# Performance work log

Measured on AMD Instinct MI355X. Metric: run time of the kernel, lower is better.

The kernel has to match this reference:

```python
import jax, jax.numpy as jnp
import numpy as np

B, Q, C, NH, NL, NP, DFF = 8, 300, 256, 8, 4, 4, 1024
DH = C // NH
SHAPES = [(100, 100), (50, 50), (25, 25), (13, 13)]  # (H, W) per level
LEN = sum(h * w for h, w in SHAPES)


def _ln(x, g, b):
    m = x.mean(-1, keepdims=True)
    v = ((x - m) ** 2).mean(-1, keepdims=True)
    return (x - m) / jnp.sqrt(v + 1e-5) * g + b


def _bilinear(v, loc, H, W):
    # v: [B, NH, H*W, DH]; loc: [B, NH, Q, NP, 2] normalized to [0,1]
    # grid_sample(align_corners=False, padding_mode='zeros') semantics
    x = loc[..., 0] * W - 0.5
    y = loc[..., 1] * H - 0.5
    x0 = jnp.floor(x)
    y0 = jnp.floor(y)
    dx = x - x0
    dy = y - y0
    out = jnp.zeros(x.shape + (v.shape[-1],), v.dtype)
    for xi, yi, wgt in ((x0, y0, (1 - dx) * (1 - dy)),
                        (x0 + 1, y0, dx * (1 - dy)),
                        (x0, y0 + 1, (1 - dx) * dy),
                        (x0 + 1, y0 + 1, dx * dy)):
        valid = ((xi >= 0) & (xi < W) & (yi >= 0) & (yi < H)).astype(v.dtype)
        idx = jnp.clip(yi, 0, H - 1).astype(jnp.int32) * W + jnp.clip(xi, 0, W - 1).astype(jnp.int32)
        g = jnp.take_along_axis(v, idx.reshape(idx.shape[0], idx.shape[1], -1)[..., None], axis=2)
        out = out + (wgt * valid)[..., None] * g.reshape(x.shape + (v.shape[-1],))
    return out


def _forward(tgt, reference_points, memory, query_pos_embed,
             Wq, bq, Wk, bk, Wv, bv, Wo, bo, g1, be1,
             W_off, b_off, W_attn, b_attn, W_val, b_val, W_out, b_out, g2, be2,
             W1, b1, W2, b2, g3, be3):
    scale = 1.0 / float(np.sqrt(DH))
    # ---- self attention (q = k = tgt + pos, v = tgt) ----
    qk = tgt + query_pos_embed
    q = (qk @ Wq + bq).reshape(B, Q, NH, DH)
    k = (qk @ Wk + bk).reshape(B, Q, NH, DH)
    v = (tgt @ Wv + bv).reshape(B, Q, NH, DH)
    attn = jax.nn.softmax(jnp.einsum('bqhd,bkhd->bhqk', q, k) * scale, axis=-1)
    sa = jnp.einsum('bhqk,bkhd->bqhd', attn, v).reshape(B, Q, C) @ Wo + bo
    t = _ln(tgt + sa, g1, be1)
    # ---- multi-scale deformable cross attention ----
    query = t + query_pos_embed
    value = (memory @ W_val + b_val).reshape(B, LEN, NH, DH).transpose(0, 2, 1, 3)  # [B,NH,LEN,DH]
    off = (query @ W_off + b_off).reshape(B, Q, NH, NL, NP, 2)
    aw = jax.nn.softmax((query @ W_attn + b_attn).reshape(B, Q, NH, NL * NP), axis=-1)
    aw = aw.reshape(B, Q, NH, NL, NP)
    wh = jnp.array([[w, h] for h, w in SHAPES], jnp.float32)  # offset normalizer (W, H)
    loc = reference_points[:, :, None, :, None, :] + off / wh[None, None, None, :, None, :]
    out = jnp.zeros((B, NH, Q, DH), t.dtype)
    start = 0
    for l, (h, w) in enumerate(SHAPES):
        v_l = value[:, :, start:start + h * w]
        loc_l = loc[:, :, :, l].transpose(0, 2, 1, 3, 4)  # [B,NH,Q,NP,2]
        samp = _bilinear(v_l, loc_l, h, w)                # [B,NH,Q,NP,DH]
        out = out + (samp * aw[:, :, :, l].transpose(0, 2, 1, 3)[..., None]).sum(3)
        start += h * w
    ca = out.transpose(0, 2, 1, 3).reshape(B, Q, C) @ W_out + b_out
    t = _ln(t + ca, g2, be2)
    # ---- FFN ----
    ff = jax.nn.relu(t @ W1 + b1) @ W2 + b2
    return _ln(t + ff, g3, be3)


def setup_inputs() -> dict:
    ks = jax.random.split(jax.random.key(0), 16)
    z, o = jnp.zeros, jnp.ones
    w = lambda i, sh: jax.random.normal(ks[i], sh, jnp.float32) * 0.02
    return {
        'tgt': jax.random.normal(ks[0], (B, Q, C), jnp.float32),
        'reference_points': jax.random.uniform(ks[1], (B, Q, NL, 2), jnp.float32),
        'memory': jax.random.normal(ks[2], (B, LEN, C), jnp.float32),
        'query_pos_embed': jax.random.normal(ks[3], (B, Q, C), jnp.float32),
        'Wq': w(4, (C, C)), 'bq': z(C), 'Wk': w(5, (C, C)), 'bk': z(C),
        'Wv': w(6, (C, C)), 'bv': z(C), 'Wo': w(7, (C, C)), 'bo': z(C),
        'g1': o(C), 'be1': z(C),
        'W_off': w(8, (C, NH * NL * NP * 2)), 'b_off': z(NH * NL * NP * 2),
        'W_attn': w(9, (C, NH * NL * NP)), 'b_attn': z(NH * NL * NP),
        'W_val': w(10, (C, C)), 'b_val': z(C), 'W_out': w(11, (C, C)), 'b_out': z(C),
        'g2': o(C), 'be2': z(C),
        'W1': w(12, (C, DFF)), 'b1': z(DFF), 'W2': w(13, (DFF, C)), 'b2': z(C),
        'g3': o(C), 'be3': z(C),
        'spatial_shapes': jnp.array(SHAPES, jnp.int32),
        'level_start_index': jnp.array(np.cumsum([0] + [h * w for h, w in SHAPES[:-1]]), jnp.int32),
    }


def reference(tgt, reference_points, memory, query_pos_embed,
              Wq, bq, Wk, bk, Wv, bv, Wo, bo, g1, be1,
              W_off, b_off, W_attn, b_attn, W_val, b_val, W_out, b_out, g2, be2,
              W1, b1, W2, b2, g3, be3, spatial_shapes, level_start_index):
    return _forward(tgt, reference_points, memory, query_pos_embed,
                    Wq, bq, Wk, bk, Wv, bv, Wo, bo, g1, be1,
                    W_off, b_off, W_attn, b_attn, W_val, b_val, W_out, b_out, g2, be2,
                    W1, b1, W2, b2, g3, be3)
```

## Files before the change

kernel.cpp:

```cpp
#include <hip/hip_runtime.h>
#include <hip/hip_bf16.h>
#include <math.h>

#define B_   8
#define Q_   300
#define C_   256
#define NH_  8
#define NL_  4
#define NP_  4
#define DFF_ 1024
#define DH_  32
#define LEN_ 13294
#define MQ_  (B_*Q_)
#define MV_  (B_*LEN_)
#define NSTRIP_ 3324

typedef __attribute__((ext_vector_type(4))) float f32x4;
typedef __attribute__((ext_vector_type(8))) short bf16x8;
typedef __hip_bfloat16 bf16;

#define GLOAD16(gp, lp) __builtin_amdgcn_global_load_lds( \
    (const __attribute__((address_space(1))) unsigned int*)(gp), \
    (__attribute__((address_space(3))) unsigned int*)(lp), 16, 0, 0)

__device__ __forceinline__ short f2bfbits(float x) {
    bf16 h = __float2bfloat16(x);
    return *reinterpret_cast<short*>(&h);
}

__global__ __launch_bounds__(256) void k_dualcvt(const float* __restrict__ tgt,
                                                 const float* __restrict__ qpe,
                                                 bf16* __restrict__ qk_o,
                                                 bf16* __restrict__ tgt_o, int n8) {
    int i = blockIdx.x * 256 + threadIdx.x;
    if (i >= n8) return;
    const float4* pa = (const float4*)(tgt + (size_t)i * 8);
    const float4* pb = (const float4*)(qpe + (size_t)i * 8);
    float4 x = pa[0], y = pa[1], u = pb[0], w = pb[1];
    union { bf16 h[8]; uint4 v; } s, t;
    s.h[0] = __float2bfloat16(x.x + u.x); s.h[1] = __float2bfloat16(x.y + u.y);
    s.h[2] = __float2bfloat16(x.z + u.z); s.h[3] = __float2bfloat16(x.w + u.w);
    s.h[4] = __float2bfloat16(y.x + w.x); s.h[5] = __float2bfloat16(y.y + w.y);
    s.h[6] = __float2bfloat16(y.z + w.z); s.h[7] = __float2bfloat16(y.w + w.w);
    t.h[0] = __float2bfloat16(x.x); t.h[1] = __float2bfloat16(x.y);
    t.h[2] = __float2bfloat16(x.z); t.h[3] = __float2bfloat16(x.w);
    t.h[4] = __float2bfloat16(y.x); t.h[5] = __float2bfloat16(y.y);
    t.h[6] = __float2bfloat16(y.z); t.h[7] = __float2bfloat16(y.w);
    *(uint4*)(qk_o + (size_t)i * 8)  = s.v;
    *(uint4*)(tgt_o + (size_t)i * 8) = t.v;
}

__global__ __launch_bounds__(256) void k_wtall(
        const float* __restrict__ Wq, const float* __restrict__ Wk,
        const float* __restrict__ Wv, const float* __restrict__ Wo,
        const float* __restrict__ Wval, const float* __restrict__ Woff,
        const float* __restrict__ Wattn, const float* __restrict__ Wout,
        const float* __restrict__ W1, const float* __restrict__ W2,
        bf16* __restrict__ Wqk_t, bf16* __restrict__ Wv_t, bf16* __restrict__ Wo_t,
        bf16* __restrict__ Wval_t, bf16* __restrict__ Woa_t, bf16* __restrict__ Wout_t,
        bf16* __restrict__ W1_t, bf16* __restrict__ W2_t) {
    __shared__ float t[32][33];
    const int id = blockIdx.x;
    const float* W; bf16* D; int K, N, r;
    if      (id < 64)  { W = Wq;    D = Wqk_t;          K = 256;  N = 256;  r = id; }
    else if (id < 128) { W = Wk;    D = Wqk_t + 65536;  K = 256;  N = 256;  r = id - 64; }
    else if (id < 192) { W = Wv;    D = Wv_t;           K = 256;  N = 256;  r = id - 128; }
    else if (id < 256) { W = Wo;    D = Wo_t;           K = 256;  N = 256;  r = id - 192; }
    else if (id < 320) { W = Wval;  D = Wval_t;         K = 256;  N = 256;  r = id - 256; }
    else if (id < 384) { W = Woff;  D = Woa_t;          K = 256;  N = 256;  r = id - 320; }
    else if (id < 416) { W = Wattn; D = Woa_t + 65536;  K = 256;  N = 128;  r = id - 384; }
    else if (id < 480) { W = Wout;  D = Wout_t;         K = 256;  N = 256;  r = id - 416; }
    else if (id < 736) { W = W1;    D = W1_t;           K = 256;  N = 1024; r = id - 480; }
    else               { W = W2;    D = W2_t;           K = 1024; N = 256;  r = id - 736; }
    const int nx = N >> 5;
    const int k0 = (r / nx) * 32, n0 = (r % nx) * 32;
    const int c = threadIdx.x & 31, rr = threadIdx.x >> 5;
#pragma unroll
    for (int i = 0; i < 4; ++i)
        t[rr + i * 8][c] = W[(size_t)(k0 + rr + i * 8) * N + n0 + c];
    __syncthreads();
#pragma unroll
    for (int i = 0; i < 4; ++i)
        D[(size_t)(n0 + rr + i * 8) * K + k0 + c] = __float2bfloat16(t[c][rr + i * 8]);
}

__global__ __launch_bounds__(256, 2) void k_gmmV(const float* __restrict__ A,
                                                 const bf16* __restrict__ Bt,
                                                 const float* __restrict__ bias,
                                                 bf16* __restrict__ outh,
                                                 int M) {
    __shared__ short As[2][8 * 32 * 32];
    const int tid = threadIdx.x;
    const int w = tid >> 6, lane = tid & 63;
    const int fr = lane & 15, fq = lane >> 4;
    const int r   = tid >> 3;
    const int itc = tid & 7;

    bf16x8 bc[4][8];
#pragma unroll
    for (int n = 0; n < 4; ++n)
#pragma unroll
        for (int it = 0; it < 8; ++it)
            bc[n][it] = *(const bf16x8*)(Bt + (size_t)(w * 64 + n * 16 + fr) * 256 + it * 32 + fq * 8);
    float bs[4];
#pragma unroll
    for (int n = 0; n < 4; ++n) bs[n] = bias[w * 64 + n * 16 + fr];

    const int sbase = blockIdx.x * 4;
    float4 pf[8];

#define LOADA(s_) { \
        int row_ = (s_) * 32 + r; if (row_ > M - 1) row_ = M - 1; \
        const float4* p_ = (const float4*)(A + (size_t)row_ * 256 + itc * 32); \
        pf[0] = p_[0]; pf[1] = p_[1]; pf[2] = p_[2]; pf[3] = p_[3]; \
        pf[4] = p_[4]; pf[5] = p_[5]; pf[6] = p_[6]; pf[7] = p_[7]; }
#define WRITEA(buf_) { \
        short* dst_ = &As[buf_][itc * 1024 + r * 32]; \
        _Pragma("unroll") \
        for (int g_ = 0; g_ < 4; ++g_) { \
            float4 a0_ = pf[2 * g_], a1_ = pf[2 * g_ + 1]; \
            union { short h[8]; bf16x8 v; } cv_; \
            cv_.h[0] = f2bfbits(a0_.x); cv_.h[1] = f2bfbits(a0_.y); \
            cv_.h[2] = f2bfbits(a0_.z); cv_.h[3] = f2bfbits(a0_.w); \
            cv_.h[4] = f2bfbits(a1_.x); cv_.h[5] = f2bfbits(a1_.y); \
            cv_.h[6] = f2bfbits(a1_.z); cv_.h[7] = f2bfbits(a1_.w); \
            *(bf16x8*)(dst_ + g_ * 8) = cv_.v; \
        } }

    LOADA(sbase);
    WRITEA(0);
    __syncthreads();
    int buf = 0;
#pragma unroll 1
    for (int i = 0; i < 4; ++i) {
        const int s = sbase + i;
        if (s >= NSTRIP_) break;
        const bool more = (i < 3) && (s + 1 < NSTRIP_);
        if (more) LOADA(s + 1);
        f32x4 acc[2][4] = {};
#pragma unroll
        for (int it = 0; it < 8; ++it) {
            bf16x8 af[2];
#pragma unroll
            for (int m = 0; m < 2; ++m)
                af[m] = *(const bf16x8*)&As[buf][it * 1024 + (m * 16 + fr) * 32 + fq * 8];
#pragma unroll
            for (int m = 0; m < 2; ++m)
#pragma unroll
                for (int n = 0; n < 4; ++n)
                    acc[m][n] = __builtin_amdgcn_mfma_f32_16x16x32_bf16(af[m], bc[n][it], acc[m][n], 0, 0, 0);
        }
        if (more) WRITEA(buf ^ 1);
#pragma unroll
        for (int m = 0; m < 2; ++m)
#pragma unroll
            for (int n = 0; n < 4; ++n) {
                const int c = w * 64 + n * 16 + fr;
#pragma unroll
                for (int j = 0; j < 4; ++j) {
                    const int row = s * 32 + m * 16 + fq * 4 + j;
                    if (row < M)
                        outh[(size_t)row * 256 + c] = __float2bfloat16(acc[m][n][j] + bs[n]);
                }
            }
        if (more) __syncthreads();
        buf ^= 1;
    }
#undef LOADA
#undef WRITEA
}

template<int RELU, int OUT_MODE>
__global__ __launch_bounds__(256) void k_gmm64(const bf16* __restrict__ A,
                                               const bf16* __restrict__ Bt,
                                               const float* __restrict__ bias0,
                                               const float* __restrict__ bias1,
                                               int nsplit,
                                               float* __restrict__ outf,
                                               bf16* __restrict__ outh,
                                               int M, int N, int K) {
    __shared__ bf16 As[64 * 32];
    __shared__ bf16 Bs[64 * 32];
    const int tid  = threadIdx.x;
    const int wid  = tid >> 6, lane = tid & 63;
    const int m0 = blockIdx.y * 64, n0 = blockIdx.x * 64;
    const int wr = wid >> 1, wc = wid & 1;
    const int fr = lane & 15, fq = lane >> 4;
    const int rloc = wid * 16 + (lane >> 2);
    const int kof  = (lane & 3) * 8;
    f32x4 acc[2][2] = {};
    for (int k0 = 0; k0 < K; k0 += 32) {
        if (k0) __syncthreads();
        int gr = m0 + rloc; if (gr > M - 1) gr = M - 1;
        GLOAD16(A + (size_t)gr * K + k0 + kof, As + rloc * 32);
        int gc = n0 + rloc; if (gc > N - 1) gc = N - 1;
        GLOAD16(Bt + (size_t)gc * K + k0 + kof, Bs + rloc * 32);
        __syncthreads();
        bf16x8 af[2], bfr[2];
#pragma unroll
        for (int m = 0; m < 2; ++m)
            af[m] = *(const bf16x8*)(As + (wr * 32 + m * 16 + fr) * 32 + fq * 8);
#pragma unroll
        for (int n = 0; n < 2; ++n)
            bfr[n] = *(const bf16x8*)(Bs + (wc * 32 + n * 16 + fr) * 32 + fq * 8);
#pragma unroll
        for (int m = 0; m < 2; ++m)
#pragma unroll
            for (int n = 0; n < 2; ++n)
                acc[m][n] = __builtin_amdgcn_mfma_f32_16x16x32_bf16(af[m], bfr[n], acc[m][n], 0, 0, 0);
    }
#pragma unroll
    for (int m = 0; m < 2; ++m) {
#pragma unroll
        for (int n = 0; n < 2; ++n) {
            const int c = n0 + wc * 32 + n * 16 + fr;
            const float bs = (c < nsplit) ? bias0[c] : bias1[c - nsplit];
#pragma unroll
            for (int j = 0; j < 4; ++j) {
                const int r = m0 + wr * 32 + m * 16 + fq * 4 + j;
                if (r >= M) continue;
                float v = acc[m][n][j] + bs;
                if (RELU) v = fmaxf(v, 0.f);
                if (OUT_MODE == 0) outf[(size_t)r * N + c] = v;
                else               outh[(size_t)r * N + c] = __float2bfloat16(v);
            }
        }
    }
}

__global__ __launch_bounds__(256) void k_attn(const bf16* __restrict__ qk2,
                                              const bf16* __restrict__ vb,
                                              bf16* __restrict__ sa) {
    __shared__ short Ks[304][40];
    __shared__ short Vt[32][328];
    __shared__ short Ps[4][16][168];
    const int tid = threadIdx.x, w = tid >> 6, lane = tid & 63;
    const int fr = lane & 15, fq = lane >> 4;
    const int bh = blockIdx.y, b = bh >> 3, h = bh & 7;
    const int qbase = blockIdx.x * 64;

    for (int k0 = 0; k0 < 300; k0 += 64) {
        int key = k0 + (tid >> 2);
        int dc = (tid & 3) * 8;
        if (key < 300) {
            *(bf16x8*)&Ks[key][dc] =
                *(const bf16x8*)&qk2[((size_t)(b * 300 + key)) * 512 + 256 + h * 32 + dc];
            bf16x8 v8 = *(const bf16x8*)&vb[((size_t)(b * 300 + key)) * 256 + h * 32 + dc];
#pragma unroll
            for (int i = 0; i < 8; ++i) Vt[dc + i][key] = v8[i];
        }
    }
    for (int i = tid; i < 32 * 20; i += 256) Vt[i & 31][300 + (i >> 5)] = 0;

    int qrow = qbase + w * 16 + fr;
    int qr = qrow < 300 ? qrow : 299;
    bf16x8 qf = *(const bf16x8*)&qk2[((size_t)(b * 300 + qr)) * 512 + h * 32 + fq * 8];
    __syncthreads();

    f32x4 s[19];
#pragma unroll
    for (int kf = 0; kf < 19; ++kf) {
        bf16x8 kfr = *(const bf16x8*)&Ks[kf * 16 + fr][fq * 8];
        f32x4 z = {};
        s[kf] = __builtin_amdgcn_mfma_f32_16x16x32_bf16(qf, kfr, z, 0, 0, 0);
    }
    const float scale = 0.17677669529663687f;
#pragma unroll
    for (int kf = 0; kf < 19; ++kf)
#pragma unroll
        for (int j = 0; j < 4; ++j) s[kf][j] *= scale;
    if (288 + fr >= 300) {
#pragma unroll
        for (int j = 0; j < 4; ++j) s[18][j] = -1e30f;
    }
    float mx[4], sm[4], inv[4];
#pragma unroll
    for (int j = 0; j < 4; ++j) {
        mx[j] = s[0][j];
#pragma unroll
        for (int kf = 1; kf < 19; ++kf) mx[j] = fmaxf(mx[j], s[kf][j]);
    }
#pragma unroll
    for (int off = 1; off < 16; off <<= 1)
#pragma unroll
        for (int j = 0; j < 4; ++j) mx[j] = fmaxf(mx[j], __shfl_xor(mx[j], off));
#pragma unroll
    for (int j = 0; j < 4; ++j) sm[j] = 0.f;
#pragma unroll
    for (int kf = 0; kf < 19; ++kf)
#pragma unroll
        for (int j = 0; j < 4; ++j) { s[kf][j] = expf(s[kf][j] - mx[j]); sm[j] += s[kf][j]; }
#pragma unroll
    for (int off = 1; off < 16; off <<= 1)
#pragma unroll
        for (int j = 0; j < 4; ++j) sm[j] += __shfl_xor(sm[j], off);
#pragma unroll
    for (int j = 0; j < 4; ++j) inv[j] = 1.f / sm[j];

    f32x4 o[2] = {};
#pragma unroll
    for (int half = 0; half < 2; ++half) {
        const int kfbeg = half * 10, kfend = half ? 19 : 10;
#pragma unroll
        for (int kf = kfbeg; kf < kfend; ++kf) {
            int gcol = kf * 16 + fr, lcol = gcol - half * 160;
            bool valid = gcol < 300;
#pragma unroll
            for (int j = 0; j < 4; ++j)
                Ps[w][fq * 4 + j][lcol] = valid ? f2bfbits(s[kf][j] * inv[j]) : (short)0;
        }
        if (half) {
            int r = lane >> 2, c0 = 144 + (lane & 3) * 4;
#pragma unroll
            for (int i = 0; i < 4; ++i) Ps[w][r][c0 + i] = 0;
        }
#pragma unroll
        for (int ks = 0; ks < 5; ++ks) {
            bf16x8 pa = *(const bf16x8*)&Ps[w][fr][ks * 32 + fq * 8];
#pragma unroll
            for (int n = 0; n < 2; ++n) {
                bf16x8 vf = *(const bf16x8*)&Vt[n * 16 + fr][half * 160 + ks * 32 + fq * 8];
                o[n] = __builtin_amdgcn_mfma_f32_16x16x32_bf16(pa, vf, o[n], 0, 0, 0);
            }
        }
    }
#pragma unroll
    for (int n = 0; n < 2; ++n)
#pragma unroll
        for (int j = 0; j < 4; ++j) {
            int row = qbase + w * 16 + fq * 4 + j;
            if (row < 300)
                sa[((size_t)(b * 300 + row)) * 256 + h * 32 + n * 16 + fr] = __float2bfloat16(o[n][j]);
        }
}

template<int WB>
__global__ __launch_bounds__(256) void k_ln(const float* __restrict__ x,
                                            const float* __restrict__ res,
                                            const float* __restrict__ qpe,
                                            const float* __restrict__ g,
                                            const float* __restrict__ be,
                                            float* __restrict__ out,
                                            bf16* __restrict__ outh, int rows) {
    const int row = blockIdx.x;
    const int tid = threadIdx.x;
    float v = x[row * C_ + tid] + res[row * C_ + tid];
    __shared__ float red[4];
    float s = v;
#pragma unroll
    for (int off = 32; off; off >>= 1) s += __shfl_xor(s, off);
    if ((tid & 63) == 0) red[tid >> 6] = s;
    __syncthreads();
    float mean = (red[0] + red[1] + red[2] + red[3]) * (1.f / C_);
    float dv = v - mean;
    float s2 = dv * dv;
    __syncthreads();
#pragma unroll
    for (int off = 32; off; off >>= 1) s2 += __shfl_xor(s2, off);
    if ((tid & 63) == 0) red[tid >> 6] = s2;
    __syncthreads();
    float var = (red[0] + red[1] + red[2] + red[3]) * (1.f / C_);
    float rstd = 1.f / sqrtf(var + 1e-5f);
    float y = dv * rstd * g[tid] + be[tid];
    out[row * C_ + tid] = y;
    if (WB == 1) outh[row * C_ + tid] = __float2bfloat16(y);
    if (WB == 2) outh[row * C_ + tid] = __float2bfloat16(y + qpe[row * C_ + tid]);
}

__global__ __launch_bounds__(256) void k_sample(const bf16* __restrict__ value,
                                                const float* __restrict__ refp,
                                                const float* __restrict__ offaw,
                                                bf16* __restrict__ out) {
    const int t  = blockIdx.x * 256 + threadIdx.x;
    const int d2 = t & 15;
    const int g  = t >> 4;
    const int h  = g & 7;
    const int bq = g >> 3;
    const int b  = bq / Q_;
    const int starts[4] = {0, 10000, 12500, 13125};
    const int HW[4]     = {100, 50, 25, 13};
    const float* offp = offaw + (size_t)bq * 384 + h * 32;

    float myl = offaw[(size_t)bq * 384 + 256 + h * 16 + d2];
    float mxl = myl;
#pragma unroll
    for (int o = 1; o < 16; o <<= 1) mxl = fmaxf(mxl, __shfl_xor(mxl, o));
    float e = expf(myl - mxl);
    float se = e;
#pragma unroll
    for (int o = 1; o < 16; o <<= 1) se += __shfl_xor(se, o);
    const float myaw = e / se;

    float acc0 = 0.f, acc1 = 0.f;
#pragma unroll
    for (int l = 0; l < NL_; ++l) {
        const int Hl = HW[l], Wl = HW[l], st = starts[l];
        const float rx = refp[(bq * NL_ + l) * 2 + 0];
        const float ry = refp[(bq * NL_ + l) * 2 + 1];
        const bf16* vbase = value + ((size_t)b * LEN_ + st) * C_ + h * DH_ + d2 * 2;
#pragma unroll
        for (int p = 0; p < NP_; ++p) {
            const float ox = offp[l * 8 + p * 2 + 0];
            const float oy = offp[l * 8 + p * 2 + 1];
            const float x = (rx + ox / (float)Wl) * (float)Wl - 0.5f;
            const float y = (ry + oy / (float)Hl) * (float)Hl - 0.5f;
            const float x0 = floorf(x), y0 = floorf(y);
            const float dx = x - x0, dy = y - y0;
            const int ix0 = (int)x0, iy0 = (int)y0;
            const float aw = __shfl(myaw, l * 4 + p, 16);
            float s0 = 0.f, s1 = 0.f;
#pragma unroll
            for (int cor = 0; cor < 4; ++cor) {
                const int xi = ix0 + (cor & 1), yi = iy0 + (cor >> 1);
                if (xi >= 0 && xi < Wl && yi >= 0 && yi < Hl) {
                    const float wg = (cor & 1 ? dx : 1.f - dx) * (cor >> 1 ? dy : 1.f - dy);
                    const unsigned u = *(const unsigned*)(vbase + (size_t)(yi * Wl + xi) * C_);
                    bf16 lo, hi;
                    *reinterpret_cast<short*>(&lo) = (short)(u & 0xFFFF);
                    *reinterpret_cast<short*>(&hi) = (short)(u >> 16);
                    s0 += wg * __bfloat162float(lo);
                    s1 += wg * __bfloat162float(hi);
                }
            }
            acc0 += aw * s0;
            acc1 += aw * s1;
        }
    }
    union { short h2[2]; unsigned u; } pack;
    pack.h2[0] = f2bfbits(acc0);
    pack.h2[1] = f2bfbits(acc1);
    *(unsigned*)(out + (size_t)bq * C_ + h * DH_ + d2 * 2) = pack.u;
}

extern "C" void kernel_launch(void* const* d_in, const int* in_sizes, int n_in,
                              void* d_out, int out_size, void* d_ws, size_t ws_size,
                              hipStream_t stream) {
    const float* tgt    = (const float*)d_in[0];
    const float* refp   = (const float*)d_in[1];
    const float* memory = (const float*)d_in[2];
    const float* qpe    = (const float*)d_in[3];
    const float* Wq     = (const float*)d_in[4];  const float* bq_  = (const float*)d_in[5];
    const float* Wk     = (const float*)d_in[6];  const float* bk_  = (const float*)d_in[7];
    const float* Wv     = (const float*)d_in[8];  const float* bv_  = (const float*)d_in[9];
    const float* Wo     = (const float*)d_in[10]; const float* bo_  = (const float*)d_in[11];
    const float* g1     = (const float*)d_in[12]; const float* be1  = (const float*)d_in[13];
    const float* W_off  = (const float*)d_in[14]; const float* b_off  = (const float*)d_in[15];
    const float* W_attn = (const float*)d_in[16]; const float* b_attn = (const float*)d_in[17];
    const float* W_val  = (const float*)d_in[18]; const float* b_val  = (const float*)d_in[19];
    const float* W_out  = (const float*)d_in[20]; const float* b_out  = (const float*)d_in[21];
    const float* g2     = (const float*)d_in[22]; const float* be2  = (const float*)d_in[23];
    const float* W1     = (const float*)d_in[24]; const float* b1   = (const float*)d_in[25];
    const float* W2     = (const float*)d_in[26]; const float* b2   = (const float*)d_in[27];
    const float* g3     = (const float*)d_in[28]; const float* be3  = (const float*)d_in[29];
    float* out = (float*)d_out;

    char* base = (char*)d_ws;
    size_t off = 0;
    auto alloc = [&](size_t bytes) -> char* {
        char* p = base + off; off = (off + bytes + 255) & ~(size_t)255; return p;
    };
    float* t1       = (float*)alloc(MQ_ * C_ * 4);
    float* offaw    = (float*)alloc((size_t)MQ_ * 384 * 4);
    bf16*  query_bf = (bf16*) alloc(MQ_ * C_ * 2);
    bf16*  dsout_bf = (bf16*) alloc(MQ_ * C_ * 2);
    bf16*  Wqk_t  = (bf16*)alloc(512 * C_ * 2);
    bf16*  Wv_t   = (bf16*)alloc(C_ * C_ * 2);
    bf16*  Wo_t   = (bf16*)alloc(C_ * C_ * 2);
    bf16*  Wval_t = (bf16*)alloc(C_ * C_ * 2);
    bf16*  Woa_t  = (bf16*)alloc(384 * C_ * 2);
    bf16*  Wout_t = (bf16*)alloc(C_ * C_ * 2);
    bf16*  W1_t   = (bf16*)alloc(C_ * DFF_ * 2);
    bf16*  W2_t   = (bf16*)alloc(DFF_ * C_ * 2);
    char*  U      = alloc((size_t)MV_ * C_ * 2);
    bf16*  qk_bf  = (bf16*)(U);
    bf16*  tgt_bf = (bf16*)(U + 1228800);
    bf16*  qkbuf  = (bf16*)(U + 2457600);
    bf16*  vb     = (bf16*)(U + 4915200);
    bf16*  sa_bf  = (bf16*)(U + 6144000);
    float* saO    = (float*)(U + 7372800);
    bf16*  value_bf = (bf16*)(U);
    float* ca     = (float*)(U);
    float* t2     = (float*)(U + 2457600);
    bf16*  t2_bf  = (bf16*) (U + 4915200);
    bf16*  ff1_bf = (bf16*) (U + 6144000);
    float* ff2    = (float*)(U + 11059200);

    k_wtall<<<992, 256, 0, stream>>>(Wq, Wk, Wv, Wo, W_val, W_off, W_attn, W_out, W1, W2,
                                     Wqk_t, Wv_t, Wo_t, Wval_t, Woa_t, Wout_t, W1_t, W2_t);
    k_dualcvt<<<300, 256, 0, stream>>>(tgt, qpe, qk_bf, tgt_bf, MQ_ * C_ / 8);

    k_gmm64<0,1><<<dim3(8, 38), 256, 0, stream>>>(qk_bf,  Wqk_t, bq_, bk_, 256, nullptr, qkbuf, MQ_, 512, C_);
    k_gmm64<0,1><<<dim3(4, 38), 256, 0, stream>>>(tgt_bf, Wv_t,  bv_, bv_, 256, nullptr, vb,    MQ_, 256, C_);
    k_attn<<<dim3(5, 64), 256, 0, stream>>>(qkbuf, vb, sa_bf);
    k_gmm64<0,0><<<dim3(4, 38), 256, 0, stream>>>(sa_bf, Wo_t, bo_, bo_, 256, saO, nullptr, MQ_, 256, C_);
    k_ln<2><<<2400, 256, 0, stream>>>(tgt, saO, qpe, g1, be1, t1, query_bf, MQ_);

    k_gmm64<0,0><<<dim3(6, 38), 256, 0, stream>>>(query_bf, Woa_t, b_off, b_attn, 256, offaw, nullptr, MQ_, 384, C_);
    k_gmmV<<<832, 256, 0, stream>>>(memory, Wval_t, b_val, value_bf, MV_);
    k_sample<<<1200, 256, 0, stream>>>(value_bf, refp, offaw, dsout_bf);
    k_gmm64<0,0><<<dim3(4, 38), 256, 0, stream>>>(dsout_bf, Wout_t, b_out, b_out, 256, ca, nullptr, MQ_, 256, C_);
    k_ln<1><<<2400, 256, 0, stream>>>(t1, ca, nullptr, g2, be2, t2, t2_bf, MQ_);

    k_gmm64<1,1><<<dim3(16, 38), 256, 0, stream>>>(t2_bf, W1_t, b1, b1, DFF_, nullptr, ff1_bf, MQ_, DFF_, C_);
    k_gmm64<0,0><<<dim3(4, 38), 256, 0, stream>>>(ff1_bf, W2_t, b2, b2, 256, ff2, nullptr, MQ_, C_, DFF_);
    k_ln<0><<<2400, 256, 0, stream>>>(t2, ff2, nullptr, g3, be3, out, nullptr, MQ_);
}
```

Baseline: 168.1 us.

## Merge independent launches into combined prep and GEMM mega-kernels

Merges the weight-transpose and input-conversion kernels into one launch, and runs the memory value projection concurrently with the QK and V projections in a single mega-kernel dispatched by block index. Value output moves to its own workspace buffer so it no longer aliases the self-attention scratch. The goal is fewer launches and better fill of the GPU by the small self-attention GEMMs. In exchange the mega-kernel sizes shared memory for the largest branch and uses launch bounds for two blocks per CU, which may limit occupancy of the small GEMM branches.

```diff
diff --git a/kernel.cpp b/kernel.cpp
--- a/kernel.cpp
+++ b/kernel.cpp
@@ -28,68 +28,65 @@
     return *reinterpret_cast<short*>(&h);
 }
 
-__global__ __launch_bounds__(256) void k_dualcvt(const float* __restrict__ tgt,
-                                                 const float* __restrict__ qpe,
-                                                 bf16* __restrict__ qk_o,
-                                                 bf16* __restrict__ tgt_o, int n8) {
-    int i = blockIdx.x * 256 + threadIdx.x;
-    if (i >= n8) return;
-    const float4* pa = (const float4*)(tgt + (size_t)i * 8);
-    const float4* pb = (const float4*)(qpe + (size_t)i * 8);
-    float4 x = pa[0], y = pa[1], u = pb[0], w = pb[1];
-    union { bf16 h[8]; uint4 v; } s, t;
-    s.h[0] = __float2bfloat16(x.x + u.x); s.h[1] = __float2bfloat16(x.y + u.y);
-    s.h[2] = __float2bfloat16(x.z + u.z); s.h[3] = __float2bfloat16(x.w + u.w);
-    s.h[4] = __float2bfloat16(y.x + w.x); s.h[5] = __float2bfloat16(y.y + w.y);
-    s.h[6] = __float2bfloat16(y.z + w.z); s.h[7] = __float2bfloat16(y.w + w.w);
-    t.h[0] = __float2bfloat16(x.x); t.h[1] = __float2bfloat16(x.y);
-    t.h[2] = __float2bfloat16(x.z); t.h[3] = __float2bfloat16(x.w);
-    t.h[4] = __float2bfloat16(y.x); t.h[5] = __float2bfloat16(y.y);
-    t.h[6] = __float2bfloat16(y.z); t.h[7] = __float2bfloat16(y.w);
-    *(uint4*)(qk_o + (size_t)i * 8)  = s.v;
-    *(uint4*)(tgt_o + (size_t)i * 8) = t.v;
-}
-
-__global__ __launch_bounds__(256) void k_wtall(
-        const float* __restrict__ Wq, const float* __restrict__ Wk,
-        const float* __restrict__ Wv, const float* __restrict__ Wo,
-        const float* __restrict__ Wval, const float* __restrict__ Woff,
-        const float* __restrict__ Wattn, const float* __restrict__ Wout,
-        const float* __restrict__ W1, const float* __restrict__ W2,
-        bf16* __restrict__ Wqk_t, bf16* __restrict__ Wv_t, bf16* __restrict__ Wo_t,
-        bf16* __restrict__ Wval_t, bf16* __restrict__ Woa_t, bf16* __restrict__ Wout_t,
-        bf16* __restrict__ W1_t, bf16* __restrict__ W2_t) {
-    __shared__ float t[32][33];
-    const int id = blockIdx.x;
-    const float* W; bf16* D; int K, N, r;
-    if      (id < 64)  { W = Wq;    D = Wqk_t;          K = 256;  N = 256;  r = id; }
-    else if (id < 128) { W = Wk;    D = Wqk_t + 65536;  K = 256;  N = 256;  r = id - 64; }
-    else if (id < 192) { W = Wv;    D = Wv_t;           K = 256;  N = 256;  r = id - 128; }
-    else if (id < 256) { W = Wo;    D = Wo_t;           K = 256;  N = 256;  r = id - 192; }
-    else if (id < 320) { W = Wval;  D = Wval_t;         K = 256;  N = 256;  r = id - 256; }
-    else if (id < 384) { W = Woff;  D = Woa_t;          K = 256;  N = 256;  r = id - 320; }
-    else if (id < 416) { W = Wattn; D = Woa_t + 65536;  K = 256;  N = 128;  r = id - 384; }
-    else if (id < 480) { W = Wout;  D = Wout_t;         K = 256;  N = 256;  r = id - 416; }
-    else if (id < 736) { W = W1;    D = W1_t;           K = 256;  N = 1024; r = id - 480; }
-    else               { W = W2;    D = W2_t;           K = 1024; N = 256;  r = id - 736; }
-    const int nx = N >> 5;
-    const int k0 = (r / nx) * 32, n0 = (r % nx) * 32;
-    const int c = threadIdx.x & 31, rr = threadIdx.x >> 5;
-#pragma unroll
-    for (int i = 0; i < 4; ++i)
-        t[rr + i * 8][c] = W[(size_t)(k0 + rr + i * 8) * N + n0 + c];
-    __syncthreads();
-#pragma unroll
-    for (int i = 0; i < 4; ++i)
-        D[(size_t)(n0 + rr + i * 8) * K + k0 + c] = __float2bfloat16(t[c][rr + i * 8]);
-}
-
-__global__ __launch_bounds__(256, 2) void k_gmmV(const float* __restrict__ A,
-                                                 const bf16* __restrict__ Bt,
-                                                 const float* __restrict__ bias,
-                                                 bf16* __restrict__ outh,
-                                                 int M) {
-    __shared__ short As[2][8 * 32 * 32];
+
+__device__ __forceinline__ void gmm64_body(char* smemraw, int bx, int by,
+        const bf16* __restrict__ A, const bf16* __restrict__ Bt,
+        const float* __restrict__ bias0, const float* __restrict__ bias1, int nsplit,
+        float* __restrict__ outf, bf16* __restrict__ outh,
+        int M, int N, int K, int RELU, int OUT_MODE) {
+    bf16* As = (bf16*)smemraw;
+    bf16* Bs = (bf16*)(smemraw + 4096);
+    const int tid  = threadIdx.x;
+    const int wid  = tid >> 6, lane = tid & 63;
+    const int m0 = by * 64, n0 = bx * 64;
+    const int wr = wid >> 1, wc = wid & 1;
+    const int fr = lane & 15, fq = lane >> 4;
+    const int rloc = wid * 16 + (lane >> 2);
+    const int kof  = (lane & 3) * 8;
+    f32x4 acc[2][2] = {};
+    for (int k0 = 0; k0 < K; k0 += 32) {
+        if (k0) __syncthreads();
+        int gr = m0 + rloc; if (gr > M - 1) gr = M - 1;
+        GLOAD16(A + (size_t)gr * K + k0 + kof, As + rloc * 32);
+        int gc = n0 + rloc; if (gc > N - 1) gc = N - 1;
+        GLOAD16(Bt + (size_t)gc * K + k0 + kof, Bs + rloc * 32);
+        __syncthreads();
+        bf16x8 af[2], bfr[2];
+#pragma unroll
+        for (int m = 0; m < 2; ++m)
+            af[m] = *(const bf16x8*)(As + (wr * 32 + m * 16 + fr) * 32 + fq * 8);
+#pragma unroll
+        for (int n = 0; n < 2; ++n)
+            bfr[n] = *(const bf16x8*)(Bs + (wc * 32 + n * 16 + fr) * 32 + fq * 8);
+#pragma unroll
+        for (int m = 0; m < 2; ++m)
+#pragma unroll
+            for (int n = 0; n < 2; ++n)
+                acc[m][n] = __builtin_amdgcn_mfma_f32_16x16x32_bf16(af[m], bfr[n], acc[m][n], 0, 0, 0);
+    }
+#pragma unroll
+    for (int m = 0; m < 2; ++m) {
+#pragma unroll
+        for (int n = 0; n < 2; ++n) {
+            const int c = n0 + wc * 32 + n * 16 + fr;
+            const float bs = (c < nsplit) ? bias0[c] : bias1[c - nsplit];
+#pragma unroll
+            for (int j = 0; j < 4; ++j) {
+                const int r = m0 + wr * 32 + m * 16 + fq * 4 + j;
+                if (r >= M) continue;
+                float v = acc[m][n][j] + bs;
+                if (RELU) v = fmaxf(v, 0.f);
+                if (OUT_MODE == 0) outf[(size_t)r * N + c] = v;
+                else               outh[(size_t)r * N + c] = __float2bfloat16(v);
+            }
+        }
+    }
+}
+
+__device__ __forceinline__ void gmmV_body(char* smemraw, int bid,
+        const float* __restrict__ A, const bf16* __restrict__ Bt,
+        const float* __restrict__ bias, bf16* __restrict__ outh, int M) {
+    short (*As)[8192] = (short(*)[8192])smemraw;
     const int tid = threadIdx.x;
     const int w = tid >> 6, lane = tid & 63;
     const int fr = lane & 15, fq = lane >> 4;
@@ -106,7 +103,7 @@
 #pragma unroll
     for (int n = 0; n < 4; ++n) bs[n] = bias[w * 64 + n * 16 + fr];
 
-    const int sbase = blockIdx.x * 4;
+    const int sbase = bid * 4;
     float4 pf[8];
 
 #define LOADA(s_) { \
@@ -170,6 +167,82 @@
 #undef WRITEA
 }
 
+
+__global__ __launch_bounds__(256) void k_prep(
+        const float* __restrict__ Wq, const float* __restrict__ Wk,
+        const float* __restrict__ Wv, const float* __restrict__ Wo,
+        const float* __restrict__ Wval, const float* __restrict__ Woff,
+        const float* __restrict__ Wattn, const float* __restrict__ Wout,
+        const float* __restrict__ W1, const float* __restrict__ W2,
+        bf16* __restrict__ Wqk_t, bf16* __restrict__ Wv_t, bf16* __restrict__ Wo_t,
+        bf16* __restrict__ Wval_t, bf16* __restrict__ Woa_t, bf16* __restrict__ Wout_t,
+        bf16* __restrict__ W1_t, bf16* __restrict__ W2_t,
+        const float* __restrict__ tgt, const float* __restrict__ qpe,
+        bf16* __restrict__ qk_o, bf16* __restrict__ tgt_o) {
+    __shared__ float t[32][33];
+    const int id = blockIdx.x;
+    if (id < 992) {
+        const float* W; bf16* D; int K, N, r;
+        if      (id < 64)  { W = Wq;    D = Wqk_t;          K = 256;  N = 256;  r = id; }
+        else if (id < 128) { W = Wk;    D = Wqk_t + 65536;  K = 256;  N = 256;  r = id - 64; }
+        else if (id < 192) { W = Wv;    D = Wv_t;           K = 256;  N = 256;  r = id - 128; }
+        else if (id < 256) { W = Wo;    D = Wo_t;           K = 256;  N = 256;  r = id - 192; }
+        else if (id < 320) { W = Wval;  D = Wval_t;         K = 256;  N = 256;  r = id - 256; }
+        else if (id < 384) { W = Woff;  D = Woa_t;          K = 256;  N = 256;  r = id - 320; }
+        else if (id < 416) { W = Wattn; D = Woa_t + 65536;  K = 256;  N = 128;  r = id - 384; }
+        else if (id < 480) { W = Wout;  D = Wout_t;         K = 256;  N = 256;  r = id - 416; }
+        else if (id < 736) { W = W1;    D = W1_t;           K = 256;  N = 1024; r = id - 480; }
+        else               { W = W2;    D = W2_t;           K = 1024; N = 256;  r = id - 736; }
+        const int nx = N >> 5;
+        const int k0 = (r / nx) * 32, n0 = (r % nx) * 32;
+        const int c = threadIdx.x & 31, rr = threadIdx.x >> 5;
+#pragma unroll
+        for (int i = 0; i < 4; ++i)
+            t[rr + i * 8][c] = W[(size_t)(k0 + rr + i * 8) * N + n0 + c];
+        __syncthreads();
+#pragma unroll
+        for (int i = 0; i < 4; ++i)
+            D[(size_t)(n0 + rr + i * 8) * K + k0 + c] = __float2bfloat16(t[c][rr + i * 8]);
+    } else {
+        const int i = (id - 992) * 256 + threadIdx.x;
+        if (i >= MQ_ * C_ / 8) return;
+        const float4* pa = (const float4*)(tgt + (size_t)i * 8);
+        const float4* pb = (const float4*)(qpe + (size_t)i * 8);
+        float4 x = pa[0], y = pa[1], u = pb[0], w = pb[1];
+        union { bf16 h[8]; uint4 v; } s, tt;
+        s.h[0] = __float2bfloat16(x.x + u.x); s.h[1] = __float2bfloat16(x.y + u.y);
+        s.h[2] = __float2bfloat16(x.z + u.z); s.h[3] = __float2bfloat16(x.w + u.w);
+        s.h[4] = __float2bfloat16(y.x + w.x); s.h[5] = __float2bfloat16(y.y + w.y);
+        s.h[6] = __float2bfloat16(y.z + w.z); s.h[7] = __float2bfloat16(y.w + w.w);
+        tt.h[0] = __float2bfloat16(x.x); tt.h[1] = __float2bfloat16(x.y);
+        tt.h[2] = __float2bfloat16(x.z); tt.h[3] = __float2bfloat16(x.w);
+        tt.h[4] = __float2bfloat16(y.x); tt.h[5] = __float2bfloat16(y.y);
+        tt.h[6] = __float2bfloat16(y.z); tt.h[7] = __float2bfloat16(y.w);
+        *(uint4*)(qk_o + (size_t)i * 8)  = s.v;
+        *(uint4*)(tgt_o + (size_t)i * 8) = tt.v;
+    }
+}
+
+__global__ __launch_bounds__(256, 2) void k_mega(
+        const float* __restrict__ memory, const bf16* __restrict__ Wval_t,
+        const float* __restrict__ b_val, bf16* __restrict__ value_bf,
+        const bf16* __restrict__ qk_bf, const bf16* __restrict__ Wqk_t,
+        const float* __restrict__ bq_, const float* __restrict__ bk_, bf16* __restrict__ qkbuf,
+        const bf16* __restrict__ tgt_bf, const bf16* __restrict__ Wv_t,
+        const float* __restrict__ bv_, bf16* __restrict__ vb) {
+    __shared__ char smem[32768];
+    const int bid = blockIdx.x;
+    if (bid < 832) {
+        gmmV_body(smem, bid, memory, Wval_t, b_val, value_bf, MV_);
+    } else if (bid < 1136) {
+        const int r = bid - 832;
+        gmm64_body(smem, r & 7, r >> 3, qk_bf, Wqk_t, bq_, bk_, 256, nullptr, qkbuf, MQ_, 512, C_, 0, 1);
+    } else {
+        const int r = bid - 1136;
+        gmm64_body(smem, r & 3, r >> 2, tgt_bf, Wv_t, bv_, bv_, 256, nullptr, vb, MQ_, 256, C_, 0, 1);
+    }
+}
+
 template<int RELU, int OUT_MODE>
 __global__ __launch_bounds__(256) void k_gmm64(const bf16* __restrict__ A,
                                                const bf16* __restrict__ Bt,
@@ -179,53 +252,9 @@
                                                float* __restrict__ outf,
                                                bf16* __restrict__ outh,
                                                int M, int N, int K) {
-    __shared__ bf16 As[64 * 32];
-    __shared__ bf16 Bs[64 * 32];
-    const int tid  = threadIdx.x;
-    const int wid  = tid >> 6, lane = tid & 63;
-    const int m0 = blockIdx.y * 64, n0 = blockIdx.x * 64;
-    const int wr = wid >> 1, wc = wid & 1;
-    const int fr = lane & 15, fq = lane >> 4;
-    const int rloc = wid * 16 + (lane >> 2);
-    const int kof  = (lane & 3) * 8;
-    f32x4 acc[2][2] = {};
-    for (int k0 = 0; k0 < K; k0 += 32) {
-        if (k0) __syncthreads();
-        int gr = m0 + rloc; if (gr > M - 1) gr = M - 1;
-        GLOAD16(A + (size_t)gr * K + k0 + kof, As + rloc * 32);
-        int gc = n0 + rloc; if (gc > N - 1) gc = N - 1;
-        GLOAD16(Bt + (size_t)gc * K + k0 + kof, Bs + rloc * 32);
-        __syncthreads();
-        bf16x8 af[2], bfr[2];
-#pragma unroll
-        for (int m = 0; m < 2; ++m)
-            af[m] = *(const bf16x8*)(As + (wr * 32 + m * 16 + fr) * 32 + fq * 8);
-#pragma unroll
-        for (int n = 0; n < 2; ++n)
-            bfr[n] = *(const bf16x8*)(Bs + (wc * 32 + n * 16 + fr) * 32 + fq * 8);
-#pragma unroll
-        for (int m = 0; m < 2; ++m)
-#pragma unroll
-            for (int n = 0; n < 2; ++n)
-                acc[m][n] = __builtin_amdgcn_mfma_f32_16x16x32_bf16(af[m], bfr[n], acc[m][n], 0, 0, 0);
-    }
-#pragma unroll
-    for (int m = 0; m < 2; ++m) {
-#pragma unroll
-        for (int n = 0; n < 2; ++n) {
-            const int c = n0 + wc * 32 + n * 16 + fr;
-            const float bs = (c < nsplit) ? bias0[c] : bias1[c - nsplit];
-#pragma unroll
-            for (int j = 0; j < 4; ++j) {
-                const int r = m0 + wr * 32 + m * 16 + fq * 4 + j;
-                if (r >= M) continue;
-                float v = acc[m][n][j] + bs;
-                if (RELU) v = fmaxf(v, 0.f);
-                if (OUT_MODE == 0) outf[(size_t)r * N + c] = v;
-                else               outh[(size_t)r * N + c] = __float2bfloat16(v);
-            }
-        }
-    }
+    __shared__ char smem[8192];
+    gmm64_body(smem, blockIdx.x, blockIdx.y, A, Bt, bias0, bias1, nsplit,
+               outf, outh, M, N, K, RELU, OUT_MODE);
 }
 
 __global__ __launch_bounds__(256) void k_attn(const bf16* __restrict__ qk2,
@@ -471,6 +500,7 @@
     bf16*  Wout_t = (bf16*)alloc(C_ * C_ * 2);
     bf16*  W1_t   = (bf16*)alloc(C_ * DFF_ * 2);
     bf16*  W2_t   = (bf16*)alloc(DFF_ * C_ * 2);
+    bf16*  value_bf = (bf16*)alloc((size_t)MV_ * C_ * 2);
     char*  U      = alloc((size_t)MV_ * C_ * 2);
     bf16*  qk_bf  = (bf16*)(U);
     bf16*  tgt_bf = (bf16*)(U + 1228800);
@@ -478,29 +508,25 @@
     bf16*  vb     = (bf16*)(U + 4915200);
     bf16*  sa_bf  = (bf16*)(U + 6144000);
     float* saO    = (float*)(U + 7372800);
-    bf16*  value_bf = (bf16*)(U);
     float* ca     = (float*)(U);
     float* t2     = (float*)(U + 2457600);
     bf16*  t2_bf  = (bf16*) (U + 4915200);
     bf16*  ff1_bf = (bf16*) (U + 6144000);
     float* ff2    = (float*)(U + 11059200);
 
-    k_wtall<<<992, 256, 0, stream>>>(Wq, Wk, Wv, Wo, W_val, W_off, W_attn, W_out, W1, W2,
-                                     Wqk_t, Wv_t, Wo_t, Wval_t, Woa_t, Wout_t, W1_t, W2_t);
-    k_dualcvt<<<300, 256, 0, stream>>>(tgt, qpe, qk_bf, tgt_bf, MQ_ * C_ / 8);
-
-    k_gmm64<0,1><<<dim3(8, 38), 256, 0, stream>>>(qk_bf,  Wqk_t, bq_, bk_, 256, nullptr, qkbuf, MQ_, 512, C_);
-    k_gmm64<0,1><<<dim3(4, 38), 256, 0, stream>>>(tgt_bf, Wv_t,  bv_, bv_, 256, nullptr, vb,    MQ_, 256, C_);
+    k_prep<<<1292, 256, 0, stream>>>(Wq, Wk, Wv, Wo, W_val, W_off, W_attn, W_out, W1, W2,
+                                     Wqk_t, Wv_t, Wo_t, Wval_t, Woa_t, Wout_t, W1_t, W2_t,
+                                     tgt, qpe, qk_bf, tgt_bf);
+    k_mega<<<1288, 256, 0, stream>>>(memory, Wval_t, b_val, value_bf,
+                                     qk_bf, Wqk_t, bq_, bk_, qkbuf,
+                                     tgt_bf, Wv_t, bv_, vb);
     k_attn<<<dim3(5, 64), 256, 0, stream>>>(qkbuf, vb, sa_bf);
     k_gmm64<0,0><<<dim3(4, 38), 256, 0, stream>>>(sa_bf, Wo_t, bo_, bo_, 256, saO, nullptr, MQ_, 256, C_);
     k_ln<2><<<2400, 256, 0, stream>>>(tgt, saO, qpe, g1, be1, t1, query_bf, MQ_);
-
     k_gmm64<0,0><<<dim3(6, 38), 256, 0, stream>>>(query_bf, Woa_t, b_off, b_attn, 256, offaw, nullptr, MQ_, 384, C_);
-    k_gmmV<<<832, 256, 0, stream>>>(memory, Wval_t, b_val, value_bf, MV_);
     k_sample<<<1200, 256, 0, stream>>>(value_bf, refp, offaw, dsout_bf);
     k_gmm64<0,0><<<dim3(4, 38), 256, 0, stream>>>(dsout_bf, Wout_t, b_out, b_out, 256, ca, nullptr, MQ_, 256, C_);
     k_ln<1><<<2400, 256, 0, stream>>>(t1, ca, nullptr, g2, be2, t2, t2_bf, MQ_);
-
     k_gmm64<1,1><<<dim3(16, 38), 256, 0, stream>>>(t2_bf, W1_t, b1, b1, DFF_, nullptr, ff1_bf, MQ_, DFF_, C_);
     k_gmm64<0,0><<<dim3(4, 38), 256, 0, stream>>>(ff1_bf, W2_t, b2, b2, 256, ff2, nullptr, MQ_, C_, DFF_);
     k_ln<0><<<2400, 256, 0, stream>>>(t2, ff2, nullptr, g3, be3, out, nullptr, MQ_);
```

New measurement: 151.4 us. 9.9% less time.
